# Kernel tuning notes

Measured on AMD Instinct MI355X. Metric: run time of the kernel, lower is better.

## Reference

```python
import jax, jax.numpy as jnp
import numpy as np
import math

B, S, D, H = 4, 2048, 1024, 16
DK = D // H

def setup_inputs() -> dict:
    key = jax.random.key(0)
    ks = jax.random.split(key, 12)
    scale = 1.0 / math.sqrt(D)
    inp = {
        "query": jax.random.normal(ks[0], (B, S, D), jnp.float32),
        "key_": jax.random.normal(ks[1], (B, S, D), jnp.float32),
        "value": jax.random.normal(ks[2], (B, S, D), jnp.float32),
        "mask": jnp.broadcast_to(jnp.tril(jnp.ones((S, S), jnp.int32)), (B, S, S)),
        "Wq": jax.random.normal(ks[3], (D, D), jnp.float32) * scale,
        "bq": jnp.zeros((D,), jnp.float32),
        "Wk": jax.random.normal(ks[4], (D, D), jnp.float32) * scale,
        "bk": jnp.zeros((D,), jnp.float32),
        "Wv": jax.random.normal(ks[5], (D, D), jnp.float32) * scale,
        "bv": jnp.zeros((D,), jnp.float32),
        "Wo": jax.random.normal(ks[6], (D, D), jnp.float32) * scale,
        "bo": jnp.zeros((D,), jnp.float32),
    }
    return inp

def reference(query, key_, value, mask, Wq, bq, Wk, bk, Wv, bv, Wo, bo):
    # Linear projections (torch Linear: x @ W^T + b), split into heads [B,H,S,DK]
    def proj(x, W, b):
        y = jnp.einsum('bsd,ed->bse', x, W) + b
        return y.reshape(B, S, H, DK).transpose(0, 2, 1, 3)
    Q = proj(query, Wq, bq)
    K = proj(key_, Wk, bk)
    V = proj(value, Wv, bv)
    # scaled dot-product attention with additive mask-fill
    scores = jnp.einsum('bhqd,bhkd->bhqk', Q, K) / math.sqrt(DK)
    scores = jnp.where(mask[:, None, :, :] == 0, jnp.float32(-1e9), scores)
    attn = jax.nn.softmax(scores, axis=-1)  # dropout p=0.0 (eval) -> identity
    ctx = jnp.einsum('bhqk,bhkd->bhqd', attn, V)
    ctx = ctx.transpose(0, 2, 1, 3).reshape(B, S, D)
    out = jnp.einsum('bsd,ed->bse', ctx, Wo) + bo
    return out
```

## Files before the change

kernel.cpp:

```cpp
#include <hip/hip_runtime.h>
#include <hip/hip_bf16.h>
#include <cstdint>
#include <cstddef>

static constexpr int kB = 4, kS = 2048, kD = 1024, kH = 16, kDK = 64;
static constexpr int kM = kB * kS;

typedef __attribute__((ext_vector_type(8))) __bf16 bf16x8;
typedef __attribute__((ext_vector_type(4))) float f32x4;

#define MFMA_BF16(a, b, c) __builtin_amdgcn_mfma_f32_16x16x32_bf16((a), (b), (c), 0, 0, 0)

#define GLDS16(gp, lp)                                                        \
  __builtin_amdgcn_global_load_lds(                                           \
      (__attribute__((address_space(1))) void*)(gp),                          \
      (__attribute__((address_space(3))) void*)(lp), 16, 0, 0)

__device__ __forceinline__ bf16x8 cvt8(const float* s, int i) {
  const float4 a = ((const float4*)s)[i * 2 + 0];
  const float4 b = ((const float4*)s)[i * 2 + 1];
  bf16x8 o;
  o[0] = (__bf16)a.x; o[1] = (__bf16)a.y; o[2] = (__bf16)a.z; o[3] = (__bf16)a.w;
  o[4] = (__bf16)b.x; o[5] = (__bf16)b.y; o[6] = (__bf16)b.z; o[7] = (__bf16)b.w;
  return o;
}

__global__ __launch_bounds__(256) void cvt_f32_bf16(
    const float* __restrict__ src, __bf16* __restrict__ dst, int n8) {
  const int i = blockIdx.x * 256 + threadIdx.x;
  if (i >= n8) return;
  ((bf16x8*)dst)[i] = cvt8(src, i);
}

__global__ __launch_bounds__(256) void cvt_act3(
    const float* __restrict__ a, const float* __restrict__ b,
    const float* __restrict__ c, __bf16* __restrict__ da,
    __bf16* __restrict__ db, __bf16* __restrict__ dc) {
  const int seg = blockIdx.x >> 12;
  const int i = (blockIdx.x & 4095) * 256 + threadIdx.x;
  const float* s = seg == 0 ? a : seg == 1 ? b : c;
  __bf16* d = seg == 0 ? da : seg == 1 ? db : dc;
  ((bf16x8*)d)[i] = cvt8(s, i);
}

__global__ __launch_bounds__(256) void cvt_w4(
    const float* __restrict__ a, const float* __restrict__ b,
    const float* __restrict__ c, const float* __restrict__ d,
    __bf16* __restrict__ da, __bf16* __restrict__ db,
    __bf16* __restrict__ dc, __bf16* __restrict__ dd) {
  const int seg = blockIdx.x >> 9;
  const int i = (blockIdx.x & 511) * 256 + threadIdx.x;
  const float* s = seg == 0 ? a : seg == 1 ? b : seg == 2 ? c : d;
  __bf16* o = seg == 0 ? da : seg == 1 ? db : seg == 2 ? dc : dd;
  ((bf16x8*)o)[i] = cvt8(s, i);
}

template <typename OutT>
__device__ __forceinline__ void gemm_core(
    const __bf16* __restrict__ A, const __bf16* __restrict__ W,
    const float* __restrict__ bias, OutT* __restrict__ out, int mode, int bid,
    __bf16* As, __bf16* Ws) {
  const int tid = threadIdx.x;
  const int wave = tid >> 6, lane = tid & 63;
  const int col = lane & 15, quad = lane >> 4;
  const int m0 = (bid & 63) * 128;
  const int n0 = (bid >> 6) * 128;
  const int wr = (wave & 1) * 64, wc = (wave >> 1) * 64;

  f32x4 acc[4][4] = {};

  int srow[4], sgo[4];
#pragma unroll
  for (int i = 0; i < 4; ++i) {
    const int s = i * 256 + tid;
    srow[i] = s >> 3;
    sgo[i] = (((s & 7) ^ ((s >> 3) & 7))) * 8;
  }
  const int g0 = ((quad) ^ (col & 7)) * 16;
  const int g1 = ((quad + 4) ^ (col & 7)) * 16;

  for (int k0 = 0; k0 < 1024; k0 += 64) {
#pragma unroll
    for (int i = 0; i < 4; ++i) {
      GLDS16(A + (size_t)(m0 + srow[i]) * 1024 + k0 + sgo[i],
             (char*)As + i * 4096 + wave * 1024);
      GLDS16(W + (size_t)(n0 + srow[i]) * 1024 + k0 + sgo[i],
             (char*)Ws + i * 4096 + wave * 1024);
    }
    __syncthreads();
#pragma unroll
    for (int h = 0; h < 2; ++h) {
      const int go = h ? g1 : g0;
      bf16x8 af[4], wf[4];
#pragma unroll
      for (int t = 0; t < 4; ++t) {
        af[t] = *(const bf16x8*)((const char*)As + (wr + t * 16 + col) * 128 + go);
        wf[t] = *(const bf16x8*)((const char*)Ws + (wc + t * 16 + col) * 128 + go);
      }
#pragma unroll
      for (int rt = 0; rt < 4; ++rt)
#pragma unroll
        for (int ct = 0; ct < 4; ++ct)
          acc[rt][ct] = MFMA_BF16(af[rt], wf[ct], acc[rt][ct]);
    }
    __syncthreads();
  }

#pragma unroll
  for (int ct = 0; ct < 4; ++ct) {
    const int n = n0 + wc + ct * 16 + col;
    const float bb = bias[n];
#pragma unroll
    for (int rt = 0; rt < 4; ++rt) {
#pragma unroll
      for (int r = 0; r < 4; ++r) {
        const int m = m0 + wr + rt * 16 + quad * 4 + r;
        const float v = acc[rt][ct][r] + bb;
        size_t idx;
        if (mode == 0) {
          idx = (size_t)m * 1024 + n;
        } else {
          const int b = m >> 11, s = m & 2047;
          const int h = n >> 6, dk = n & 63;
          if (mode == 1)
            idx = ((size_t)(b * 16 + h) * 2048 + s) * 64 + dk;
          else
            idx = ((size_t)(b * 16 + h) * 64 + dk) * 2048 + s;
        }
        out[idx] = (OutT)v;
      }
    }
  }
}

template <int MODE, typename OutT>
__global__ __launch_bounds__(256) void gemm_one(
    const __bf16* __restrict__ A, const __bf16* __restrict__ W,
    const float* __restrict__ bias, OutT* __restrict__ out) {
  __shared__ __align__(16) __bf16 As[128 * 64];
  __shared__ __align__(16) __bf16 Ws[128 * 64];
  gemm_core<OutT>(A, W, bias, out, MODE, blockIdx.x, As, Ws);
}

__global__ __launch_bounds__(256) void gemm_qkv(
    const __bf16* __restrict__ Aq, const __bf16* __restrict__ Ak,
    const __bf16* __restrict__ Av, const __bf16* __restrict__ Wqb,
    const __bf16* __restrict__ Wkb, const __bf16* __restrict__ Wvb,
    const float* __restrict__ bq, const float* __restrict__ bk,
    const float* __restrict__ bv, __bf16* __restrict__ Qw,
    __bf16* __restrict__ Kw, __bf16* __restrict__ Vw) {
  __shared__ __align__(16) __bf16 As[128 * 64];
  __shared__ __align__(16) __bf16 Ws[128 * 64];
  const int seg = blockIdx.x >> 9;
  const int bid = blockIdx.x & 511;
  const __bf16* A = seg == 0 ? Aq : seg == 1 ? Ak : Av;
  const __bf16* W = seg == 0 ? Wqb : seg == 1 ? Wkb : Wvb;
  const float* bias = seg == 0 ? bq : seg == 1 ? bk : bv;
  __bf16* out = seg == 0 ? Qw : seg == 1 ? Kw : Vw;
  gemm_core<__bf16>(A, W, bias, out, seg == 2 ? 2 : 1, bid, As, Ws);
}

__global__ __launch_bounds__(256, 4) void flash_attn(
    const __bf16* __restrict__ Q, const __bf16* __restrict__ K,
    const __bf16* __restrict__ Vt, __bf16* __restrict__ ctx) {
  __shared__ __align__(16) __bf16 Ks[64 * 64];
  __shared__ __align__(16) __bf16 Vs[64 * 64];
  __shared__ __align__(16) __bf16 Pb[4][2][16 * 72];

  const int tid = threadIdx.x;
  const int wave = tid >> 6, lane = tid & 63;
  const int col = lane & 15, quad = lane >> 4;
  const int bh = blockIdx.x >> 4;
  const int pair = blockIdx.x & 15;
  const int b = bh >> 4, h = bh & 15;
  const int t_lo = pair, t_hi = 31 - pair;
  const int q0f[2] = {t_lo * 64 + wave * 16, t_hi * 64 + wave * 16};

  constexpr float SCL = 0.18033688011112042f;

  bf16x8 qf[2][2];
#pragma unroll
  for (int f = 0; f < 2; ++f) {
    const __bf16* Qp = Q + ((size_t)bh * kS + q0f[f] + col) * 64 + quad * 8;
    qf[f][0] = *(const bf16x8*)Qp;
    qf[f][1] = *(const bf16x8*)(Qp + 32);
  }

  f32x4 o[2][4] = {};
  f32x4 lacc[2] = {};
  bf16x8 ones;
#pragma unroll
  for (int i = 0; i < 8; ++i) ones[i] = (__bf16)1.0f;

  const __bf16* Kg = K + (size_t)bh * kS * 64;
  const __bf16* Vg = Vt + (size_t)bh * 64 * kS;

  const int row0 = tid >> 3, g0 = (tid & 7) ^ (row0 & 7);
  const int row1 = (256 + tid) >> 3, g1 = (tid & 7) ^ (row1 & 7);
  char* KsB = (char*)Ks + wave * 1024;
  char* VsB = (char*)Vs + wave * 1024;

  const int fgoff0 = ((quad) ^ (col & 7)) * 16;
  const int fgoff1 = ((quad + 4) ^ (col & 7)) * 16;
  const int maskbase = wave * 16 + quad * 4;

  __bf16* Pw0 = &Pb[wave][0][0];
  __bf16* Pw1 = &Pb[wave][1][0];
  const __bf16* Pr0 = Pw0 + col * 72 + quad * 8;
  const __bf16* Pr1 = Pw1 + col * 72 + quad * 8;

  auto body = [&](int c, bool lo, bool d0, bool d1) {
    const int k0 = c * 64;
    GLDS16(Kg + (size_t)(k0 + row0) * 64 + g0 * 8, KsB);
    GLDS16(Vg + (size_t)row0 * kS + k0 + g0 * 8, VsB);
    GLDS16(Kg + (size_t)(k0 + row1) * 64 + g1 * 8, KsB + 4096);
    GLDS16(Vg + (size_t)row1 * kS + k0 + g1 * 8, VsB + 4096);
    __syncthreads();

    f32x4 s[2][4];
#pragma unroll
    for (int kt = 0; kt < 4; ++kt) {
      const char* kp = (const char*)Ks + (kt * 16 + col) * 128;
      const bf16x8 kf0 = *(const bf16x8*)(kp + fgoff0);
      const bf16x8 kf1 = *(const bf16x8*)(kp + fgoff1);
      f32x4 z = {};
      s[1][kt] = MFMA_BF16(qf[1][1], kf1, MFMA_BF16(qf[1][0], kf0, z));
      if (lo) s[0][kt] = MFMA_BF16(qf[0][1], kf1, MFMA_BF16(qf[0][0], kf0, z));
    }
#pragma unroll
    for (int kt = 0; kt < 4; ++kt) {
#pragma unroll
      for (int r = 0; r < 4; ++r) {
        float pv1 = __builtin_amdgcn_exp2f(s[1][kt][r] * SCL);
        if (d1 && (kt * 16 + col > maskbase + r)) pv1 = 0.0f;
        Pw1[(quad * 4 + r) * 72 + kt * 16 + col] = (__bf16)pv1;
        if (lo) {
          float pv0 = __builtin_amdgcn_exp2f(s[0][kt][r] * SCL);
          if (d0 && (kt * 16 + col > maskbase + r)) pv0 = 0.0f;
          Pw0[(quad * 4 + r) * 72 + kt * 16 + col] = (__bf16)pv0;
        }
      }
    }
    __threadfence_block();
    const bf16x8 pf1a = *(const bf16x8*)Pr1;
    const bf16x8 pf1b = *(const bf16x8*)(Pr1 + 32);
    bf16x8 pf0a = {}, pf0b = {};
    if (lo) {
      pf0a = *(const bf16x8*)Pr0;
      pf0b = *(const bf16x8*)(Pr0 + 32);
    }
#pragma unroll
    for (int dt = 0; dt < 4; ++dt) {
      const char* vp = (const char*)Vs + (dt * 16 + col) * 128;
      const bf16x8 vf0 = *(const bf16x8*)(vp + fgoff0);
      const bf16x8 vf1 = *(const bf16x8*)(vp + fgoff1);
      o[1][dt] = MFMA_BF16(pf1b, vf1, MFMA_BF16(pf1a, vf0, o[1][dt]));
      if (lo) o[0][dt] = MFMA_BF16(pf0b, vf1, MFMA_BF16(pf0a, vf0, o[0][dt]));
    }
    lacc[1] = MFMA_BF16(pf1b, ones, MFMA_BF16(pf1a, ones, lacc[1]));
    if (lo) lacc[0] = MFMA_BF16(pf0b, ones, MFMA_BF16(pf0a, ones, lacc[0]));
    __syncthreads();
  };

  for (int c = 0; c <= t_lo; ++c) body(c, true, c == t_lo, false);
  for (int c = t_lo + 1; c <= t_hi; ++c) body(c, false, false, c == t_hi);

#pragma unroll
  for (int f = 0; f < 2; ++f) {
#pragma unroll
    for (int r = 0; r < 4; ++r) {
      const float inv = 1.0f / lacc[f][r];
      const int srow = q0f[f] + quad * 4 + r;
      __bf16* cp = ctx + ((size_t)b * kS + srow) * kD + h * 64 + col;
#pragma unroll
      for (int dt = 0; dt < 4; ++dt)
        cp[dt * 16] = (__bf16)(o[f][dt][r] * inv);
    }
  }
}

extern "C" void kernel_launch(void* const* d_in, const int* in_sizes, int n_in,
                              void* d_out, int out_size, void* d_ws, size_t ws_size,
                              hipStream_t stream) {
  const float* query = (const float*)d_in[0];
  const float* key_  = (const float*)d_in[1];
  const float* value = (const float*)d_in[2];
  const float* Wq = (const float*)d_in[4];
  const float* bq = (const float*)d_in[5];
  const float* Wk = (const float*)d_in[6];
  const float* bk = (const float*)d_in[7];
  const float* Wv = (const float*)d_in[8];
  const float* bv = (const float*)d_in[9];
  const float* Wo = (const float*)d_in[10];
  const float* bo = (const float*)d_in[11];

  const size_t e = (size_t)kM * kD;
  const size_t w = (size_t)kD * kD;
  float* out = (float*)d_out;

  const size_t REQ = (6 * e + 4 * w) * sizeof(__bf16);

  if (ws_size >= REQ) {
    __bf16* Qw  = (__bf16*)d_ws;
    __bf16* Kw  = Qw + e;
    __bf16* Vw  = Kw + e;
    __bf16* Aq  = Vw + e;
    __bf16* Ak  = Aq + e;
    __bf16* Av  = Ak + e;
    __bf16* Wqb = Av + e;
    __bf16* Wkb = Wqb + w;
    __bf16* Wvb = Wkb + w;
    __bf16* Wob = Wvb + w;

    cvt_act3<<<3 * 4096, 256, 0, stream>>>(query, key_, value, Aq, Ak, Av);
    cvt_w4<<<4 * 512, 256, 0, stream>>>(Wq, Wk, Wv, Wo, Wqb, Wkb, Wvb, Wob);
    gemm_qkv<<<1536, 256, 0, stream>>>(Aq, Ak, Av, Wqb, Wkb, Wvb, bq, bk, bv,
                                       Qw, Kw, Vw);
    flash_attn<<<kB * kH * 16, 256, 0, stream>>>(Qw, Kw, Vw, Aq);
    gemm_one<0, float><<<512, 256, 0, stream>>>(Aq, Wob, bo, out);
  } else {
    __bf16* Qw = (__bf16*)d_ws;
    __bf16* Kw = Qw + e;
    __bf16* Vw = Kw + e;
    __bf16* Ab = Vw + e;
    __bf16* Wb = Ab + e;

    const int actg = (int)(e / 8 / 256);
    const int wg = (int)(w / 8 / 256);
    cvt_f32_bf16<<<actg, 256, 0, stream>>>(query, Ab, (int)(e / 8));
    cvt_f32_bf16<<<wg, 256, 0, stream>>>(Wq, Wb, (int)(w / 8));
    gemm_one<1, __bf16><<<512, 256, 0, stream>>>(Ab, Wb, bq, Qw);
    cvt_f32_bf16<<<actg, 256, 0, stream>>>(key_, Ab, (int)(e / 8));
    cvt_f32_bf16<<<wg, 256, 0, stream>>>(Wk, Wb, (int)(w / 8));
    gemm_one<1, __bf16><<<512, 256, 0, stream>>>(Ab, Wb, bk, Kw);
    cvt_f32_bf16<<<actg, 256, 0, stream>>>(value, Ab, (int)(e / 8));
    cvt_f32_bf16<<<wg, 256, 0, stream>>>(Wv, Wb, (int)(w / 8));
    gemm_one<2, __bf16><<<512, 256, 0, stream>>>(Ab, Wb, bv, Vw);
    flash_attn<<<kB * kH * 16, 256, 0, stream>>>(Qw, Kw, Vw, Ab);
    cvt_f32_bf16<<<wg, 256, 0, stream>>>(Wo, Wb, (int)(w / 8));
    gemm_one<0, float><<<512, 256, 0, stream>>>(Ab, Wb, bo, out);
  }
}
```

Measured before the change: 354.0 us.

## Replace QKV projection GEMM with 256x256-tile, 8-wave double-buffered pipelined kernel

Swaps the 128x128-tile QKV projection kernel for a new 512-thread kernel that computes 256x256 output tiles. It double-buffers LDS with direct global-to-LDS loads, interleaved with MFMA quadrants under barriers and priority hints. Block indices are remapped so consecutive blocks are spread across XCD-like groups. This raises arithmetic intensity and overlaps loads with compute, at the cost of 128KB LDS per block, more registers for accumulators, and fewer blocks (384) for the machine.

```diff
diff --git a/kernel.cpp b/kernel.cpp
--- a/kernel.cpp
+++ b/kernel.cpp
@@ -142,23 +142,148 @@
   gemm_core<OutT>(A, W, bias, out, MODE, blockIdx.x, As, Ws);
 }
 
-__global__ __launch_bounds__(256) void gemm_qkv(
+#define READQ(B_, QM_, QN_)                                                   \
+  do {                                                                        \
+    const char* Ab_ = (const char*)As8 + ((B_) * 2 + (QM_)) * 16384 + rowA;   \
+    const char* Bb_ = (const char*)Bs8 + ((B_) * 2 + (QN_)) * 16384 + rowB;   \
+    _Pragma("unroll") for (int mi = 0; mi < 4; ++mi) {                        \
+      af[mi][0] = *(const bf16x8*)(Ab_ + mi * 2048 + gb0);                    \
+      af[mi][1] = *(const bf16x8*)(Ab_ + mi * 2048 + gb1);                    \
+    }                                                                         \
+    _Pragma("unroll") for (int ni = 0; ni < 2; ++ni) {                        \
+      bfrag[ni][0] = *(const bf16x8*)(Bb_ + ni * 2048 + gb0);                 \
+      bfrag[ni][1] = *(const bf16x8*)(Bb_ + ni * 2048 + gb1);                 \
+    }                                                                         \
+  } while (0)
+
+#define MFMAQ(QM_, QN_)                                                       \
+  do {                                                                        \
+    __builtin_amdgcn_s_barrier();                                             \
+    asm volatile("s_waitcnt lgkmcnt(0)" ::: "memory");                        \
+    __builtin_amdgcn_s_setprio(1);                                            \
+    _Pragma("unroll") for (int mi = 0; mi < 4; ++mi) {                        \
+      _Pragma("unroll") for (int ni = 0; ni < 2; ++ni) {                      \
+        f32x4& a_ = acc[(QM_) * 4 + mi][(QN_) * 2 + ni];                      \
+        a_ = MFMA_BF16(af[mi][0], bfrag[ni][0], a_);                          \
+        a_ = MFMA_BF16(af[mi][1], bfrag[ni][1], a_);                          \
+      }                                                                       \
+    }                                                                         \
+    __builtin_amdgcn_s_setprio(0);                                            \
+    __builtin_amdgcn_s_barrier();                                             \
+  } while (0)
+
+#define STAGE_A8(B_, H_, KT_)                                                 \
+  do {                                                                        \
+    char* d_ = (char*)As8 + ((B_) * 2 + (H_)) * 16384 + wave * 1024;          \
+    GLDS16(A + (size_t)(m0 + (H_) * 128 + srow) * 1024 + (KT_) * 64 + sgo,    \
+           d_);                                                               \
+    GLDS16(A + (size_t)(m0 + (H_) * 128 + 64 + srow) * 1024 + (KT_) * 64 +    \
+               sgo,                                                           \
+           d_ + 8192);                                                        \
+  } while (0)
+
+#define STAGE_B8(B_, H_, KT_)                                                 \
+  do {                                                                        \
+    char* d_ = (char*)Bs8 + ((B_) * 2 + (H_)) * 16384 + wave * 1024;          \
+    GLDS16(W + (size_t)(n0 + (H_) * 128 + srow) * 1024 + (KT_) * 64 + sgo,    \
+           d_);                                                               \
+    GLDS16(W + (size_t)(n0 + (H_) * 128 + 64 + srow) * 1024 + (KT_) * 64 +    \
+               sgo,                                                           \
+           d_ + 8192);                                                        \
+  } while (0)
+
+__global__ __launch_bounds__(512, 2) void gemm_qkv8(
     const __bf16* __restrict__ Aq, const __bf16* __restrict__ Ak,
     const __bf16* __restrict__ Av, const __bf16* __restrict__ Wqb,
     const __bf16* __restrict__ Wkb, const __bf16* __restrict__ Wvb,
     const float* __restrict__ bq, const float* __restrict__ bk,
     const float* __restrict__ bv, __bf16* __restrict__ Qw,
     __bf16* __restrict__ Kw, __bf16* __restrict__ Vw) {
-  __shared__ __align__(16) __bf16 As[128 * 64];
-  __shared__ __align__(16) __bf16 Ws[128 * 64];
-  const int seg = blockIdx.x >> 9;
-  const int bid = blockIdx.x & 511;
-  const __bf16* A = seg == 0 ? Aq : seg == 1 ? Ak : Av;
-  const __bf16* W = seg == 0 ? Wqb : seg == 1 ? Wkb : Wvb;
-  const float* bias = seg == 0 ? bq : seg == 1 ? bk : bv;
-  __bf16* out = seg == 0 ? Qw : seg == 1 ? Kw : Vw;
-  gemm_core<__bf16>(A, W, bias, out, seg == 2 ? 2 : 1, bid, As, Ws);
-}
+  __shared__ __align__(16) __bf16 As8[2][2][128 * 64];
+  __shared__ __align__(16) __bf16 Bs8[2][2][128 * 64];
+
+  int bid = (blockIdx.x & 7) * 48 + (blockIdx.x >> 3);
+  const int seg = bid >> 7;
+  bid &= 127;
+  const int m0 = (bid & 31) * 256;
+  const int n0 = (bid >> 5) * 256;
+
+  const __bf16* __restrict__ A = seg == 0 ? Aq : seg == 1 ? Ak : Av;
+  const __bf16* __restrict__ W = seg == 0 ? Wqb : seg == 1 ? Wkb : Wvb;
+  const float* __restrict__ bias = seg == 0 ? bq : seg == 1 ? bk : bv;
+  __bf16* __restrict__ out = seg == 0 ? Qw : seg == 1 ? Kw : Vw;
+  const int mode = (seg == 2) ? 2 : 1;
+
+  const int tid = threadIdx.x;
+  const int wave = tid >> 6, lane = tid & 63;
+  const int col = lane & 15, quad = lane >> 4;
+  const int wm = wave >> 2, wn = wave & 3;
+
+  const int srow = tid >> 3;
+  const int sgo = ((tid & 7) ^ (srow & 7)) * 8;
+  const int gb0 = ((quad) ^ (col & 7)) * 16;
+  const int gb1 = ((quad + 4) ^ (col & 7)) * 16;
+  const int rowA = (wm * 64 + col) * 128;
+  const int rowB = (wn * 32 + col) * 128;
+
+  f32x4 acc[8][4] = {};
+  bf16x8 af[4][2], bfrag[2][2];
+
+  STAGE_A8(0, 0, 0);
+  STAGE_B8(0, 0, 0);
+  STAGE_A8(0, 1, 0);
+  STAGE_B8(0, 1, 0);
+  STAGE_A8(1, 0, 1);
+  STAGE_B8(1, 0, 1);
+  asm volatile("s_waitcnt vmcnt(4)" ::: "memory");
+  __builtin_amdgcn_s_barrier();
+
+#pragma unroll 2
+  for (int t = 0; t < 16; ++t) {
+    const int buf = t & 1;
+    READQ(buf, 0, 0);
+    if (t < 15)
+      STAGE_A8(buf ^ 1, 1, t + 1);
+    else
+      asm volatile("s_waitcnt vmcnt(0)" ::: "memory");
+    MFMAQ(0, 0);
+    READQ(buf, 0, 1);
+    if (t < 15) STAGE_B8(buf ^ 1, 1, t + 1);
+    MFMAQ(0, 1);
+    READQ(buf, 1, 0);
+    if (t < 14) STAGE_A8(buf, 0, t + 2);
+    MFMAQ(1, 0);
+    READQ(buf, 1, 1);
+    if (t < 14) STAGE_B8(buf, 0, t + 2);
+    asm volatile("s_waitcnt vmcnt(4)" ::: "memory");
+    MFMAQ(1, 1);
+  }
+
+#pragma unroll
+  for (int an = 0; an < 4; ++an) {
+    const int n = n0 + (an >> 1) * 128 + wn * 32 + (an & 1) * 16 + col;
+    const float bb = bias[n];
+    const int hh = n >> 6, dk = n & 63;
+#pragma unroll
+    for (int am = 0; am < 8; ++am) {
+#pragma unroll
+      for (int r = 0; r < 4; ++r) {
+        const int m =
+            m0 + (am >> 2) * 128 + wm * 64 + (am & 3) * 16 + quad * 4 + r;
+        const int b_ = m >> 11, s_ = m & 2047;
+        const size_t idx =
+            (mode == 1) ? ((size_t)(b_ * 16 + hh) * 2048 + s_) * 64 + dk
+                        : ((size_t)(b_ * 16 + hh) * 64 + dk) * 2048 + s_;
+        out[idx] = (__bf16)(acc[am][an][r] + bb);
+      }
+    }
+  }
+}
+
+#undef READQ
+#undef MFMAQ
+#undef STAGE_A8
+#undef STAGE_B8
 
 __global__ __launch_bounds__(256, 4) void flash_attn(
     const __bf16* __restrict__ Q, const __bf16* __restrict__ K,
@@ -314,7 +439,7 @@
 
     cvt_act3<<<3 * 4096, 256, 0, stream>>>(query, key_, value, Aq, Ak, Av);
     cvt_w4<<<4 * 512, 256, 0, stream>>>(Wq, Wk, Wv, Wo, Wqb, Wkb, Wvb, Wob);
-    gemm_qkv<<<1536, 256, 0, stream>>>(Aq, Ak, Av, Wqb, Wkb, Wvb, bq, bk, bv,
+    gemm_qkv8<<<384, 512, 0, stream>>>(Aq, Ak, Av, Wqb, Wkb, Wvb, bq, bk, bv,
                                        Qw, Kw, Vw);
     flash_attn<<<kB * kH * 16, 256, 0, stream>>>(Qw, Kw, Vw, Aq);
     gemm_one<0, float><<<512, 256, 0, stream>>>(Aq, Wob, bo, out);
```

Measured after the change: 403.6 us. 14.0% more time.

## Double-buffer K/V tiles in flash attention and merge conversion kernels

Applied to the files above, without the earlier changes.

The flash attention kernel now keeps two LDS buffers for K and V. It issues the async global-to-LDS loads for the next key tile before computing on the current one, and waits with explicit vmcnt counts and raw s_barrier instead of __syncthreads. This is meant to hide global load latency behind the MFMA work. The launch bound drops from 4 to 3 blocks per CU to fit the extra LDS. Separately, the two fp32-to-bf16 conversion launches are merged into one kernel to save a launch.

```diff
diff --git a/kernel.cpp b/kernel.cpp
--- a/kernel.cpp
+++ b/kernel.cpp
@@ -32,27 +32,29 @@
   ((bf16x8*)dst)[i] = cvt8(src, i);
 }
 
-__global__ __launch_bounds__(256) void cvt_act3(
-    const float* __restrict__ a, const float* __restrict__ b,
-    const float* __restrict__ c, __bf16* __restrict__ da,
-    __bf16* __restrict__ db, __bf16* __restrict__ dc) {
-  const int seg = blockIdx.x >> 12;
-  const int i = (blockIdx.x & 4095) * 256 + threadIdx.x;
-  const float* s = seg == 0 ? a : seg == 1 ? b : c;
-  __bf16* d = seg == 0 ? da : seg == 1 ? db : dc;
-  ((bf16x8*)d)[i] = cvt8(s, i);
-}
-
-__global__ __launch_bounds__(256) void cvt_w4(
-    const float* __restrict__ a, const float* __restrict__ b,
-    const float* __restrict__ c, const float* __restrict__ d,
-    __bf16* __restrict__ da, __bf16* __restrict__ db,
-    __bf16* __restrict__ dc, __bf16* __restrict__ dd) {
-  const int seg = blockIdx.x >> 9;
-  const int i = (blockIdx.x & 511) * 256 + threadIdx.x;
-  const float* s = seg == 0 ? a : seg == 1 ? b : seg == 2 ? c : d;
-  __bf16* o = seg == 0 ? da : seg == 1 ? db : seg == 2 ? dc : dd;
-  ((bf16x8*)o)[i] = cvt8(s, i);
+__global__ __launch_bounds__(256) void cvt_all(
+    const float* __restrict__ q, const float* __restrict__ k,
+    const float* __restrict__ v, const float* __restrict__ wq,
+    const float* __restrict__ wk, const float* __restrict__ wv,
+    const float* __restrict__ wo, __bf16* __restrict__ dq,
+    __bf16* __restrict__ dk, __bf16* __restrict__ dv,
+    __bf16* __restrict__ dwq, __bf16* __restrict__ dwk,
+    __bf16* __restrict__ dwv, __bf16* __restrict__ dwo) {
+  int bi = blockIdx.x;
+  if (bi < 3 * 4096) {
+    const int seg = bi >> 12;
+    const int i = (bi & 4095) * 256 + threadIdx.x;
+    const float* s = seg == 0 ? q : seg == 1 ? k : v;
+    __bf16* d = seg == 0 ? dq : seg == 1 ? dk : dv;
+    ((bf16x8*)d)[i] = cvt8(s, i);
+  } else {
+    bi -= 3 * 4096;
+    const int seg = bi >> 9;
+    const int i = (bi & 511) * 256 + threadIdx.x;
+    const float* s = seg == 0 ? wq : seg == 1 ? wk : seg == 2 ? wv : wo;
+    __bf16* d = seg == 0 ? dwq : seg == 1 ? dwk : seg == 2 ? dwv : dwo;
+    ((bf16x8*)d)[i] = cvt8(s, i);
+  }
 }
 
 template <typename OutT>
@@ -160,11 +162,11 @@
   gemm_core<__bf16>(A, W, bias, out, seg == 2 ? 2 : 1, bid, As, Ws);
 }
 
-__global__ __launch_bounds__(256, 4) void flash_attn(
+__global__ __launch_bounds__(256, 3) void flash_attn(
     const __bf16* __restrict__ Q, const __bf16* __restrict__ K,
     const __bf16* __restrict__ Vt, __bf16* __restrict__ ctx) {
-  __shared__ __align__(16) __bf16 Ks[64 * 64];
-  __shared__ __align__(16) __bf16 Vs[64 * 64];
+  __shared__ __align__(16) __bf16 Ks[2][64 * 64];
+  __shared__ __align__(16) __bf16 Vs[2][64 * 64];
   __shared__ __align__(16) __bf16 Pb[4][2][16 * 72];
 
   const int tid = threadIdx.x;
@@ -197,8 +199,6 @@
 
   const int row0 = tid >> 3, g0 = (tid & 7) ^ (row0 & 7);
   const int row1 = (256 + tid) >> 3, g1 = (tid & 7) ^ (row1 & 7);
-  char* KsB = (char*)Ks + wave * 1024;
-  char* VsB = (char*)Vs + wave * 1024;
 
   const int fgoff0 = ((quad) ^ (col & 7)) * 16;
   const int fgoff1 = ((quad + 4) ^ (col & 7)) * 16;
@@ -209,18 +209,33 @@
   const __bf16* Pr0 = Pw0 + col * 72 + quad * 8;
   const __bf16* Pr1 = Pw1 + col * 72 + quad * 8;
 
-  auto body = [&](int c, bool lo, bool d0, bool d1) {
+  auto stage = [&](int c, int buf) {
     const int k0 = c * 64;
+    char* KsB = (char*)Ks + buf * 8192 + wave * 1024;
+    char* VsB = (char*)Vs + buf * 8192 + wave * 1024;
     GLDS16(Kg + (size_t)(k0 + row0) * 64 + g0 * 8, KsB);
     GLDS16(Vg + (size_t)row0 * kS + k0 + g0 * 8, VsB);
     GLDS16(Kg + (size_t)(k0 + row1) * 64 + g1 * 8, KsB + 4096);
     GLDS16(Vg + (size_t)row1 * kS + k0 + g1 * 8, VsB + 4096);
-    __syncthreads();
+  };
+
+  auto body = [&](int c, bool lo, bool d0, bool d1, bool stage_next) {
+    if (stage_next) {
+      stage(c + 1, (c + 1) & 1);
+      asm volatile("s_waitcnt vmcnt(4)" ::: "memory");
+    } else {
+      asm volatile("s_waitcnt vmcnt(0)" ::: "memory");
+    }
+    __builtin_amdgcn_s_barrier();
+    asm volatile("" ::: "memory");
+
+    const char* Ksb = (const char*)Ks + (c & 1) * 8192;
+    const char* Vsb = (const char*)Vs + (c & 1) * 8192;
 
     f32x4 s[2][4];
 #pragma unroll
     for (int kt = 0; kt < 4; ++kt) {
-      const char* kp = (const char*)Ks + (kt * 16 + col) * 128;
+      const char* kp = Ksb + (kt * 16 + col) * 128;
       const bf16x8 kf0 = *(const bf16x8*)(kp + fgoff0);
       const bf16x8 kf1 = *(const bf16x8*)(kp + fgoff1);
       f32x4 z = {};
@@ -251,7 +266,7 @@
     }
 #pragma unroll
     for (int dt = 0; dt < 4; ++dt) {
-      const char* vp = (const char*)Vs + (dt * 16 + col) * 128;
+      const char* vp = Vsb + (dt * 16 + col) * 128;
       const bf16x8 vf0 = *(const bf16x8*)(vp + fgoff0);
       const bf16x8 vf1 = *(const bf16x8*)(vp + fgoff1);
       o[1][dt] = MFMA_BF16(pf1b, vf1, MFMA_BF16(pf1a, vf0, o[1][dt]));
@@ -259,11 +274,15 @@
     }
     lacc[1] = MFMA_BF16(pf1b, ones, MFMA_BF16(pf1a, ones, lacc[1]));
     if (lo) lacc[0] = MFMA_BF16(pf0b, ones, MFMA_BF16(pf0a, ones, lacc[0]));
-    __syncthreads();
+
+    __builtin_amdgcn_s_barrier();
+    asm volatile("" ::: "memory");
   };
 
-  for (int c = 0; c <= t_lo; ++c) body(c, true, c == t_lo, false);
-  for (int c = t_lo + 1; c <= t_hi; ++c) body(c, false, false, c == t_hi);
+  stage(0, 0);
+  for (int c = 0; c <= t_lo; ++c) body(c, true, c == t_lo, false, c < t_hi);
+  for (int c = t_lo + 1; c <= t_hi; ++c)
+    body(c, false, false, c == t_hi, c < t_hi);
 
 #pragma unroll
   for (int f = 0; f < 2; ++f) {
@@ -312,8 +331,8 @@
     __bf16* Wvb = Wkb + w;
     __bf16* Wob = Wvb + w;
 
-    cvt_act3<<<3 * 4096, 256, 0, stream>>>(query, key_, value, Aq, Ak, Av);
-    cvt_w4<<<4 * 512, 256, 0, stream>>>(Wq, Wk, Wv, Wo, Wqb, Wkb, Wvb, Wob);
+    cvt_all<<<3 * 4096 + 4 * 512, 256, 0, stream>>>(
+        query, key_, value, Wq, Wk, Wv, Wo, Aq, Ak, Av, Wqb, Wkb, Wvb, Wob);
     gemm_qkv<<<1536, 256, 0, stream>>>(Aq, Ak, Av, Wqb, Wkb, Wvb, bq, bk, bv,
                                        Qw, Kw, Vw);
     flash_attn<<<kB * kH * 16, 256, 0, stream>>>(Qw, Kw, Vw, Aq);
```

After: 364.8 us. +3.1%, slower.
